# Optimization experiments

Measured on AMD Instinct MI355X. Metric: run time of the kernel, lower is better.

The kernel has to match this reference:

```python
import jax, jax.numpy as jnp
import numpy as np

EPS = 1e-6

def setup_inputs() -> dict:
    key = jax.random.key(0)
    kq, kk, kv = jax.random.split(key, 3)
    B, H, S, D = 4, 16, 2048, 64
    q = jax.random.normal(kq, (B, H, S, D), dtype=jnp.float32)
    k = jax.random.normal(kk, (B, H, S, D), dtype=jnp.float32)
    v = jax.random.normal(kv, (B, H, S, D), dtype=jnp.float32)
    return {"q": q, "k": k, "v": v}

def reference(q, k, v):
    # ReBASED parallel attention: squared QK^T scores, causal mask, sum-normalized.
    scale = q.shape[-1] ** (-0.5)
    q = q * scale
    # attn: [B, H, S, S]
    attn = jnp.einsum('bhqd,bhkd->bhqk', q, k)
    attn = attn * attn  # squared scores
    S = q.shape[-2]
    causal = jnp.tril(jnp.ones((S, S), dtype=bool))
    attn = jnp.where(causal, attn, 0.0)
    o = jnp.einsum('bhqk,bhkd->bhqd', attn, v)
    z = attn.sum(-1, keepdims=True)
    return o / (z + EPS)
```

## Files before the change

kernel.cpp:

```cpp
#include <hip/hip_runtime.h>
#include <hip/hip_bf16.h>


#define SEQ 2048
#define HD  64
#define BQ  128
#define BK  64
#define LQ  72
#define LV  76

typedef __attribute__((ext_vector_type(8))) short bf16x8;
typedef __attribute__((ext_vector_type(4))) short bf16x4;
typedef __attribute__((ext_vector_type(4))) float f32x4;

__device__ inline unsigned packbf(float a, float b) {
    __hip_bfloat162 h = __float22bfloat162_rn(make_float2(a, b));
    union { __hip_bfloat162 h2; unsigned u; } cv; cv.h2 = h; return cv.u;
}

__global__ __launch_bounds__(256, 2)
void rebased_r3_kernel(const float* __restrict__ qg,
                       const float* __restrict__ kg,
                       const float* __restrict__ vg,
                       float* __restrict__ og) {
    __shared__ __align__(16) unsigned short Qs[BQ][LQ];
    __shared__ __align__(16) unsigned short Ks[2][BK][LQ];
    __shared__ __align__(16) unsigned short Vst[2][HD][LV];

    const int t    = threadIdx.x;
    const int lane = t & 63;
    const int w    = t >> 6;
    const int li   = lane & 15;
    const int qd   = lane >> 4;
    const int pj   = blockIdx.x;
    const int head = blockIdx.y;
    const size_t base = (size_t)head * SEQ * HD;

    #pragma unroll
    for (int seg = 0; seg < 2; ++seg) {
        const int qt = seg ? pj : (15 - pj);
        const int ktmax = 2 * qt + 1;

        float4 qreg[8], kreg[4], vreg[4];
        {
            const float4* qsrc = (const float4*)(qg + base + (size_t)qt * BQ * HD);
            #pragma unroll
            for (int l = 0; l < 8; ++l) qreg[l] = qsrc[t + l * 256];
            const float4* ksrc = (const float4*)(kg + base);
            const float4* vsrc = (const float4*)(vg + base);
            #pragma unroll
            for (int l = 0; l < 4; ++l) kreg[l] = ksrc[t + l * 256];
            const int d4g = t & 15, rp = t >> 4;
            #pragma unroll
            for (int p = 0; p < 2; ++p) {
                int r0 = p * 32 + rp * 2;
                vreg[2 * p]     = vsrc[r0 * 16 + d4g];
                vreg[2 * p + 1] = vsrc[(r0 + 1) * 16 + d4g];
            }
        }
        __syncthreads();

        #pragma unroll
        for (int l = 0; l < 8; ++l) {
            int f = t + l * 256, row = f >> 4, d4 = (f & 15) << 2;
            unsigned* dst = (unsigned*)&Qs[row][d4];
            dst[0] = packbf(qreg[l].x * 0.125f, qreg[l].y * 0.125f);
            dst[1] = packbf(qreg[l].z * 0.125f, qreg[l].w * 0.125f);
        }
        #pragma unroll
        for (int l = 0; l < 4; ++l) {
            int row = (t >> 4) + l * 16, d4 = (t & 15) << 2;
            unsigned* dst = (unsigned*)&Ks[0][row][d4];
            dst[0] = packbf(kreg[l].x, kreg[l].y);
            dst[1] = packbf(kreg[l].z, kreg[l].w);
        }
        {
            const int d4g = t & 15, rp = t >> 4;
            #pragma unroll
            for (int p = 0; p < 2; ++p) {
                int r0 = p * 32 + rp * 2;
                float a0[4] = {vreg[2*p].x, vreg[2*p].y, vreg[2*p].z, vreg[2*p].w};
                float a1[4] = {vreg[2*p+1].x, vreg[2*p+1].y, vreg[2*p+1].z, vreg[2*p+1].w};
                #pragma unroll
                for (int j = 0; j < 4; ++j)
                    *(unsigned*)&Vst[0][d4g * 4 + j][r0] = packbf(a0[j], a1[j]);
            }
        }
        __syncthreads();

        f32x4 oacc[2][4];
        float zpart[2] = {0.f, 0.f};
        #pragma unroll
        for (int mt = 0; mt < 2; ++mt)
            #pragma unroll
            for (int nd = 0; nd < 4; ++nd) oacc[mt][nd] = (f32x4){0.f, 0.f, 0.f, 0.f};

        for (int kt = 0; kt <= ktmax; ++kt) {
            const int cur = kt & 1;

            if (kt < ktmax) {
                const float4* ksrc = (const float4*)(kg + base + (size_t)(kt + 1) * BK * HD);
                const float4* vsrc = (const float4*)(vg + base + (size_t)(kt + 1) * BK * HD);
                #pragma unroll
                for (int l = 0; l < 4; ++l) kreg[l] = ksrc[t + l * 256];
                const int d4g = t & 15, rp = t >> 4;
                #pragma unroll
                for (int p = 0; p < 2; ++p) {
                    int r0 = p * 32 + rp * 2;
                    vreg[2 * p]     = vsrc[r0 * 16 + d4g];
                    vreg[2 * p + 1] = vsrc[(r0 + 1) * 16 + d4g];
                }
            }

            const int qrow_min = qt * BQ + w * 32;
            const bool active   = (kt * BK <= qrow_min + 31);
            const bool needmask = (kt * BK + 63 > qrow_min);

            if (active) {
                f32x4 stt[4][2];
                #pragma unroll
                for (int nk = 0; nk < 4; ++nk)
                    #pragma unroll
                    for (int mt = 0; mt < 2; ++mt) stt[nk][mt] = (f32x4){0.f,0.f,0.f,0.f};
                #pragma unroll
                for (int ks = 0; ks < 2; ++ks) {
                    const int kb = ks * 32 + qd * 8;
                    bf16x8 kf[4], qf[2];
                    #pragma unroll
                    for (int nk = 0; nk < 4; ++nk)
                        kf[nk] = *(const bf16x8*)&Ks[cur][nk * 16 + li][kb];
                    #pragma unroll
                    for (int mt = 0; mt < 2; ++mt)
                        qf[mt] = *(const bf16x8*)&Qs[w * 32 + mt * 16 + li][kb];
                    #pragma unroll
                    for (int nk = 0; nk < 4; ++nk)
                        #pragma unroll
                        for (int mt = 0; mt < 2; ++mt)
                            stt[nk][mt] = __builtin_amdgcn_mfma_f32_16x16x32_bf16(
                                kf[nk], qf[mt], stt[nk][mt], 0, 0, 0);
                }

                unsigned pk[4][2][2];
                #pragma unroll
                for (int nk = 0; nk < 4; ++nk) {
                    const int kcb = kt * BK + nk * 16 + qd * 4;
                    #pragma unroll
                    for (int mt = 0; mt < 2; ++mt) {
                        const int qrow = qrow_min + mt * 16 + li;
                        float p[4];
                        #pragma unroll
                        for (int r = 0; r < 4; ++r) {
                            float s = stt[nk][mt][r];
                            if (needmask && (kcb + r > qrow)) s = 0.f;
                            p[r] = s * s;
                        }
                        zpart[mt] += (p[0] + p[1]) + (p[2] + p[3]);
                        pk[nk][mt][0] = packbf(p[0], p[1]);
                        pk[nk][mt][1] = packbf(p[2], p[3]);
                    }
                }

                #pragma unroll
                for (int ks16 = 0; ks16 < 4; ++ks16) {
                    bf16x4 av[2];
                    #pragma unroll
                    for (int mt = 0; mt < 2; ++mt) {
                        union { unsigned u[2]; bf16x4 v; } cv;
                        cv.u[0] = pk[ks16][mt][0]; cv.u[1] = pk[ks16][mt][1];
                        av[mt] = cv.v;
                    }
                    #pragma unroll
                    for (int nd = 0; nd < 4; ++nd) {
                        bf16x4 vf = *(const bf16x4*)&Vst[cur][nd * 16 + li][ks16 * 16 + qd * 4];
                        #pragma unroll
                        for (int mt = 0; mt < 2; ++mt)
                            oacc[mt][nd] = __builtin_amdgcn_mfma_f32_16x16x16bf16_1k(
                                av[mt], vf, oacc[mt][nd], 0, 0, 0);
                    }
                }
            }

            if (kt < ktmax) {
                const int nb = cur ^ 1;
                #pragma unroll
                for (int l = 0; l < 4; ++l) {
                    int row = (t >> 4) + l * 16, d4 = (t & 15) << 2;
                    unsigned* dst = (unsigned*)&Ks[nb][row][d4];
                    dst[0] = packbf(kreg[l].x, kreg[l].y);
                    dst[1] = packbf(kreg[l].z, kreg[l].w);
                }
                const int d4g = t & 15, rp = t >> 4;
                #pragma unroll
                for (int p = 0; p < 2; ++p) {
                    int r0 = p * 32 + rp * 2;
                    float a0[4] = {vreg[2*p].x, vreg[2*p].y, vreg[2*p].z, vreg[2*p].w};
                    float a1[4] = {vreg[2*p+1].x, vreg[2*p+1].y, vreg[2*p+1].z, vreg[2*p+1].w};
                    #pragma unroll
                    for (int j = 0; j < 4; ++j)
                        *(unsigned*)&Vst[nb][d4g * 4 + j][r0] = packbf(a0[j], a1[j]);
                }
            }
            __syncthreads();
        }

        float* odst = og + base + (size_t)qt * BQ * HD;
        #pragma unroll
        for (int mt = 0; mt < 2; ++mt) {
            float zf = zpart[mt];
            zf += __shfl_xor(zf, 16, 64);
            zf += __shfl_xor(zf, 32, 64);
            #pragma unroll
            for (int r = 0; r < 4; ++r) {
                float zr = __shfl(zf, qd * 4 + r, 64);
                float inv = 1.f / (zr + 1e-6f);
                int row = w * 32 + mt * 16 + qd * 4 + r;
                #pragma unroll
                for (int nd = 0; nd < 4; ++nd)
                    odst[row * HD + nd * 16 + li] = oacc[mt][nd][r] * inv;
            }
        }
    }
}

extern "C" void kernel_launch(void* const* d_in, const int* in_sizes, int n_in,
                              void* d_out, int out_size, void* d_ws, size_t ws_size,
                              hipStream_t stream) {
    const float* q = (const float*)d_in[0];
    const float* k = (const float*)d_in[1];
    const float* v = (const float*)d_in[2];
    float* out = (float*)d_out;

    dim3 grid(8, 64);
    dim3 block(256);
    rebased_r3_kernel<<<grid, block, 0, stream>>>(q, k, v, out);
}
```

Measured before the change: 208.7 us.

## Hold Q fragments in registers, drop Q shared tile, raise occupancy

Each wave now loads its own Q rows straight from global memory, scales them, converts them to bf16 MFMA fragments and keeps them in registers for the whole key loop. This removes the Q shared-memory tile and its per-iteration LDS reads. The change is meant to cut LDS traffic and footprint, and launch bounds go from 2 to 4 blocks per SM. The grid is also transposed so that consecutive blocks cover different heads, which changes the dispatch order. In exchange the kernel carries more live registers under a tighter register budget, so spills are possible.

```diff
diff --git a/kernel.cpp b/kernel.cpp
--- a/kernel.cpp
+++ b/kernel.cpp
@@ -18,12 +18,11 @@
     union { __hip_bfloat162 h2; unsigned u; } cv; cv.h2 = h; return cv.u;
 }
 
-__global__ __launch_bounds__(256, 2)
-void rebased_r3_kernel(const float* __restrict__ qg,
+__global__ __launch_bounds__(256, 4)
+void rebased_r4_kernel(const float* __restrict__ qg,
                        const float* __restrict__ kg,
                        const float* __restrict__ vg,
                        float* __restrict__ og) {
-    __shared__ __align__(16) unsigned short Qs[BQ][LQ];
     __shared__ __align__(16) unsigned short Ks[2][BK][LQ];
     __shared__ __align__(16) unsigned short Vst[2][HD][LV];
 
@@ -32,8 +31,8 @@
     const int w    = t >> 6;
     const int li   = lane & 15;
     const int qd   = lane >> 4;
-    const int pj   = blockIdx.x;
-    const int head = blockIdx.y;
+    const int head = blockIdx.x;
+    const int pj   = blockIdx.y;
     const size_t base = (size_t)head * SEQ * HD;
 
     #pragma unroll
@@ -41,11 +40,28 @@
         const int qt = seg ? pj : (15 - pj);
         const int ktmax = 2 * qt + 1;
 
-        float4 qreg[8], kreg[4], vreg[4];
+        bf16x8 qf[2][2];
         {
-            const float4* qsrc = (const float4*)(qg + base + (size_t)qt * BQ * HD);
-            #pragma unroll
-            for (int l = 0; l < 8; ++l) qreg[l] = qsrc[t + l * 256];
+            const int qrow0 = qt * BQ + w * 32;
+            #pragma unroll
+            for (int mt = 0; mt < 2; ++mt) {
+                const float* qrow = qg + base + (size_t)(qrow0 + mt * 16 + li) * HD;
+                #pragma unroll
+                for (int ks = 0; ks < 2; ++ks) {
+                    float4 a = *(const float4*)(qrow + ks * 32 + qd * 8);
+                    float4 b = *(const float4*)(qrow + ks * 32 + qd * 8 + 4);
+                    union { unsigned u[4]; bf16x8 v; } cv;
+                    cv.u[0] = packbf(a.x * 0.125f, a.y * 0.125f);
+                    cv.u[1] = packbf(a.z * 0.125f, a.w * 0.125f);
+                    cv.u[2] = packbf(b.x * 0.125f, b.y * 0.125f);
+                    cv.u[3] = packbf(b.z * 0.125f, b.w * 0.125f);
+                    qf[ks][mt] = cv.v;
+                }
+            }
+        }
+
+        float4 kreg[4], vreg[4];
+        {
             const float4* ksrc = (const float4*)(kg + base);
             const float4* vsrc = (const float4*)(vg + base);
             #pragma unroll
@@ -60,13 +76,6 @@
         }
         __syncthreads();
 
-        #pragma unroll
-        for (int l = 0; l < 8; ++l) {
-            int f = t + l * 256, row = f >> 4, d4 = (f & 15) << 2;
-            unsigned* dst = (unsigned*)&Qs[row][d4];
-            dst[0] = packbf(qreg[l].x * 0.125f, qreg[l].y * 0.125f);
-            dst[1] = packbf(qreg[l].z * 0.125f, qreg[l].w * 0.125f);
-        }
         #pragma unroll
         for (int l = 0; l < 4; ++l) {
             int row = (t >> 4) + l * 16, d4 = (t & 15) << 2;
@@ -125,19 +134,16 @@
                 #pragma unroll
                 for (int ks = 0; ks < 2; ++ks) {
                     const int kb = ks * 32 + qd * 8;
-                    bf16x8 kf[4], qf[2];
+                    bf16x8 kf[4];
                     #pragma unroll
                     for (int nk = 0; nk < 4; ++nk)
                         kf[nk] = *(const bf16x8*)&Ks[cur][nk * 16 + li][kb];
-                    #pragma unroll
-                    for (int mt = 0; mt < 2; ++mt)
-                        qf[mt] = *(const bf16x8*)&Qs[w * 32 + mt * 16 + li][kb];
                     #pragma unroll
                     for (int nk = 0; nk < 4; ++nk)
                         #pragma unroll
                         for (int mt = 0; mt < 2; ++mt)
                             stt[nk][mt] = __builtin_amdgcn_mfma_f32_16x16x32_bf16(
-                                kf[nk], qf[mt], stt[nk][mt], 0, 0, 0);
+                                kf[nk], qf[ks][mt], stt[nk][mt], 0, 0, 0);
                 }
 
                 unsigned pk[4][2][2];
@@ -230,7 +236,7 @@
     const float* v = (const float*)d_in[2];
     float* out = (float*)d_out;
 
-    dim3 grid(8, 64);
+    dim3 grid(64, 8);
     dim3 block(256);
-    rebased_r3_kernel<<<grid, block, 0, stream>>>(q, k, v, out);
+    rebased_r4_kernel<<<grid, block, 0, stream>>>(q, k, v, out);
 }
```

New measurement: 415.1 us. +98.9%, slower.
